# Kernel tuning notes

Hardware: AMD Instinct MI355X
Metric: run time of the kernel (lower is better)

The kernel has to match this reference:

```python
import jax, jax.numpy as jnp
import numpy as np

N, FIN, H, FOUT = 4096, 128, 4, 64
NEG_INF = -1e9


def _xavier(key, shape):
    fan_in, fan_out = shape[-2], shape[-1]
    limit = float(np.sqrt(6.0 / (fan_in + fan_out)))
    return jax.random.uniform(key, shape, jnp.float32, -limit, limit)


def setup_inputs() -> dict:
    key = jax.random.key(0)
    ks = jax.random.split(key, 7)
    x = jax.random.normal(ks[0], (N, FIN), jnp.float32)
    u = jax.random.uniform(ks[1], (N, N))
    mask = jnp.where(u < 0.02, 0.0, NEG_INF).astype(jnp.float32)
    idx = jnp.arange(N)
    mask = mask.at[idx, idx].set(0.0)
    proj_param = _xavier(ks[2], (H, FIN, FOUT))          # per-head projection
    score_src = _xavier(ks[3], (H, FOUT, 1))             # scoring_fn_source (IMP1 layout)
    score_tgt = _xavier(ks[4], (H, FOUT, 1))             # scoring_fn_target
    skip_w = _xavier(ks[5], (H * FOUT, FIN))             # skip_proj Linear weight
    bias = jnp.zeros((H * FOUT,), jnp.float32)
    return {"x": x, "mask": mask, "proj_param": proj_param,
            "score_src": score_src, "score_tgt": score_tgt,
            "skip_w": skip_w, "bias": bias}


def reference(x, mask, proj_param, score_src, score_tgt, skip_w, bias):
    # project: [1,N,Fin] @ [H,Fin,Fout] -> [H,N,Fout]
    h = jnp.einsum('nf,hfo->hno', x, proj_param)
    # additive (Bahdanau-style) scores
    s_src = jnp.matmul(h, score_src)                     # [H,N,1]
    s_tgt = jnp.matmul(h, score_tgt)                     # [H,N,1]
    all_scores = jax.nn.leaky_relu(s_src + jnp.swapaxes(s_tgt, 1, 2), 0.2)  # [H,N,N]
    attn = jax.nn.softmax(all_scores + mask[None, :, :], axis=-1)           # [H,N,N]
    # aggregate: [H,N,N] @ [H,N,Fout] -> [N,H,Fout]
    out = jnp.einsum('hnm,hmo->nho', attn, h)
    # skip connection (dims differ: Fin != H*Fout -> use skip_proj)
    out = out + jnp.matmul(x, skip_w.T).reshape(N, H, FOUT)
    out = out.reshape(N, H * FOUT) + bias                # concat heads + bias
    return jax.nn.elu(out)
```

## Files before the change

kernel.cpp:

```cpp
#include <hip/hip_runtime.h>
#include <hip/hip_bf16.h>
#include <math.h>


#define NN   4096
#define FIN  128
#define NH   4
#define FO   64
#define HF   256
#define SEG  96
#define LIST 192
#define GEMM_BLOCKS 512

typedef unsigned short ushort_t;
typedef unsigned int uint4n __attribute__((ext_vector_type(4)));

__device__ __forceinline__ ushort_t f2bf(float f) {
    __hip_bfloat16 h = __float2bfloat16(f);
    union { __hip_bfloat16 h; ushort_t u; } c; c.h = h; return c.u;
}
__device__ __forceinline__ float bf2f(ushort_t u) {
    union { unsigned int i; float f; } c; c.i = ((unsigned int)u) << 16; return c.f;
}

__global__ __launch_bounds__(256) void k0_gemm(
        const float* __restrict__ x,
        const float* __restrict__ proj,
        const float* __restrict__ skw,
        const float* __restrict__ asrc,
        const float* __restrict__ atgt,
        ushort_t* __restrict__ h2b, float* __restrict__ skip_ws,
        float* __restrict__ src4, float* __restrict__ tgt4) {
    __shared__ float sA[64 * 68];
    __shared__ float sB[64 * 64];
    const int tid = threadIdx.x;
    const int blk = blockIdx.x;

    const int bc = blk >> 6;
    const int i0 = (blk & 63) * 64;
    const int tx = tid & 15, ty = tid >> 4;
    const int r0 = ty << 2, c0 = tx << 2;
    float acc[4][4] = {};

    #pragma unroll
    for (int kb = 0; kb < FIN; kb += 64) {
        if (kb) __syncthreads();
        #pragma unroll
        for (int q = 0; q < 4; q++) {
            int s   = tid + q * 256;
            int row = s >> 4;
            int c4  = (s & 15) << 2;
            float4 v = *(const float4*)(x + (size_t)(i0 + row) * FIN + kb + c4);
            float* d = sA + row * 68 + c4;
            d[0] = v.x; d[1] = v.y; d[2] = v.z; d[3] = v.w;
        }
        if (bc < 4) {
            const float4* src = (const float4*)(proj + (size_t)bc * FIN * FO
                                                + (size_t)kb * FO);
            #pragma unroll
            for (int q = 0; q < 4; q++) {
                int s = tid + q * 256;
                *(float4*)(sB + (size_t)s * 4) = src[s];
            }
        } else {
            const float* sw = skw + (size_t)(bc - 4) * 64 * FIN;
            #pragma unroll
            for (int q = 0; q < 4; q++) {
                int s  = tid + q * 256;
                int c  = s & 63;
                int k4 = (s >> 6) << 2;
                float4 v = *(const float4*)(sw + (size_t)c * FIN + kb + k4);
                sB[(k4 + 0) * 64 + c] = v.x;
                sB[(k4 + 1) * 64 + c] = v.y;
                sB[(k4 + 2) * 64 + c] = v.z;
                sB[(k4 + 3) * 64 + c] = v.w;
            }
        }
        __syncthreads();

        #pragma unroll 2
        for (int k = 0; k < 64; k += 4) {
            alignas(16) float a[4][4];
            alignas(16) float b[4][4];
            #pragma unroll
            for (int rr = 0; rr < 4; rr++)
                *(float4*)a[rr] = *(const float4*)(sA + (r0 + rr) * 68 + k);
            #pragma unroll
            for (int kk = 0; kk < 4; kk++)
                *(float4*)b[kk] = *(const float4*)(sB + (k + kk) * 64 + c0);
            #pragma unroll
            for (int kk = 0; kk < 4; kk++)
                #pragma unroll
                for (int rr = 0; rr < 4; rr++)
                    #pragma unroll
                    for (int cc = 0; cc < 4; cc++)
                        acc[rr][cc] = fmaf(a[rr][kk], b[kk][cc], acc[rr][cc]);
        }
    }

    if (bc < 4) {
        #pragma unroll
        for (int rr = 0; rr < 4; rr++) {
            ushort4 hv;
            hv.x = f2bf(acc[rr][0]); hv.y = f2bf(acc[rr][1]);
            hv.z = f2bf(acc[rr][2]); hv.w = f2bf(acc[rr][3]);
            *(ushort4*)(h2b + (size_t)(i0 + r0 + rr) * HF + bc * 64 + c0) = hv;
        }
        float as[4], at[4];
        #pragma unroll
        for (int cc = 0; cc < 4; cc++) {
            as[cc] = asrc[bc * FO + c0 + cc];
            at[cc] = atgt[bc * FO + c0 + cc];
        }
        #pragma unroll
        for (int rr = 0; rr < 4; rr++) {
            float ps = acc[rr][0] * as[0] + acc[rr][1] * as[1]
                     + acc[rr][2] * as[2] + acc[rr][3] * as[3];
            float pt = acc[rr][0] * at[0] + acc[rr][1] * at[1]
                     + acc[rr][2] * at[2] + acc[rr][3] * at[3];
            #pragma unroll
            for (int off = 8; off >= 1; off >>= 1) {
                ps += __shfl_xor(ps, off, 64);
                pt += __shfl_xor(pt, off, 64);
            }
            if (tx == 0) {
                int i = i0 + r0 + rr;
                src4[(size_t)i * 4 + bc] = ps;
                tgt4[(size_t)i * 4 + bc] = pt;
            }
        }
    } else {
        float* dst = skip_ws + (size_t)i0 * HF + (bc - 4) * 64;
        #pragma unroll
        for (int rr = 0; rr < 4; rr++)
            *(float4*)(dst + (size_t)(r0 + rr) * HF + c0) = *(float4*)acc[rr];
    }
}

__global__ __launch_bounds__(256) void k1_attn(
        const unsigned int* __restrict__ mask,
        const ushort_t* __restrict__ h2b,
        const float* __restrict__ skip_ws,
        const float* __restrict__ src4,
        const float* __restrict__ tgt4,
        const float* __restrict__ bias,
        float* __restrict__ out) {
    __shared__ ushort_t s_seg[4][SEG];
    __shared__ int      s_j[LIST];
    __shared__ float    s_p[4][LIST + 1];
    __shared__ float    s_red[4][256];
    __shared__ int      s_cnt[4];
    __shared__ float    s_inv[4];

    const int tid  = threadIdx.x;
    const int lane = tid & 63, w = tid >> 6;
    const int i    = blockIdx.x;

    const uint4n* mb = (const uint4n*)mask + (size_t)i * 1024;
    uint4n cur[4];
    #pragma unroll
    for (int s = 0; s < 4; s++)
        cur[s] = mb[w * 256 + lane + s * 64];

    const float skipv = skip_ws[(size_t)i * HF + tid];
    const float bv    = bias[tid];
    const float sc    = src4[(size_t)i * 4 + w];

    int base = 0;
    #pragma unroll
    for (int s = 0; s < 4; s++) {
        #pragma unroll
        for (int e = 0; e < 4; e++) {
            bool hit = (cur[s][e] & 0x7fffffffu) == 0u;
            unsigned long long bal = __ballot(hit);
            int pre = __builtin_amdgcn_mbcnt_hi(
                          (unsigned int)(bal >> 32),
                          __builtin_amdgcn_mbcnt_lo((unsigned int)bal, 0));
            if (hit) {
                int slot = base + pre;
                if (slot < SEG)
                    s_seg[w][slot] =
                        (ushort_t)(w * 1024 + s * 256 + lane * 4 + e);
            }
            base += (int)__popcll(bal);
        }
    }
    if (lane == 0) s_cnt[w] = base < SEG ? base : SEG;
    __syncthreads();

    const int t0 = s_cnt[0], t1 = s_cnt[1], t2 = s_cnt[2], t3 = s_cnt[3];
    const int off  = (w > 0 ? t0 : 0) + (w > 1 ? t1 : 0) + (w > 2 ? t2 : 0);
    const int mine = s_cnt[w];
    for (int kk = lane; kk < mine; kk += 64) {
        int pp = off + kk;
        if (pp < LIST) s_j[pp] = s_seg[w][kk];
    }
    int c = t0 + t1 + t2 + t3;
    c = c < LIST ? c : LIST;
    __syncthreads();

    float lsum = 0.f;
    for (int kk = lane; kk < c; kk += 64) {
        int j = s_j[kk];
        float p = sc + tgt4[(size_t)j * 4 + w];
        p = p > 0.f ? p : 0.2f * p;
        p = __expf(p);
        s_p[w][kk] = p;
        lsum += p;
    }
    #pragma unroll
    for (int o = 32; o >= 1; o >>= 1)
        lsum += __shfl_xor(lsum, o, 64);
    if (lane == 0) s_inv[w] = lsum > 0.f ? 1.0f / lsum : 0.0f;
    __syncthreads();

    const int h = lane >> 4;
    const ushort_t* hp = h2b + 4 * lane;
    float4 acc = {0.f, 0.f, 0.f, 0.f};
    int kk = w;
    for (; kk + 4 < c; kk += 8) {
        int   j0 = s_j[kk],        j1 = s_j[kk + 4];
        float p0 = s_p[h][kk],     p1 = s_p[h][kk + 4];
        ushort4 a0 = *(const ushort4*)(hp + (size_t)j0 * HF);
        ushort4 a1 = *(const ushort4*)(hp + (size_t)j1 * HF);
        acc.x = fmaf(p0, bf2f(a0.x), acc.x);
        acc.y = fmaf(p0, bf2f(a0.y), acc.y);
        acc.z = fmaf(p0, bf2f(a0.z), acc.z);
        acc.w = fmaf(p0, bf2f(a0.w), acc.w);
        acc.x = fmaf(p1, bf2f(a1.x), acc.x);
        acc.y = fmaf(p1, bf2f(a1.y), acc.y);
        acc.z = fmaf(p1, bf2f(a1.z), acc.z);
        acc.w = fmaf(p1, bf2f(a1.w), acc.w);
    }
    if (kk < c) {
        int   j0 = s_j[kk];
        float p0 = s_p[h][kk];
        ushort4 a0 = *(const ushort4*)(hp + (size_t)j0 * HF);
        acc.x = fmaf(p0, bf2f(a0.x), acc.x);
        acc.y = fmaf(p0, bf2f(a0.y), acc.y);
        acc.z = fmaf(p0, bf2f(a0.z), acc.z);
        acc.w = fmaf(p0, bf2f(a0.w), acc.w);
    }
    *(float4*)&s_red[w][4 * lane] = acc;
    __syncthreads();

    float tot = s_red[0][tid] + s_red[1][tid] + s_red[2][tid] + s_red[3][tid];
    float vv = tot * s_inv[tid >> 6] + skipv + bv;
    vv = vv > 0.f ? vv : expm1f(vv);
    out[(size_t)i * HF + tid] = vv;
}

extern "C" void kernel_launch(void* const* d_in, const int* in_sizes, int n_in,
                              void* d_out, int out_size, void* d_ws, size_t ws_size,
                              hipStream_t stream) {
    const float*        x    = (const float*)d_in[0];
    const unsigned int* mask = (const unsigned int*)d_in[1];
    const float*        proj = (const float*)d_in[2];
    const float*        asrc = (const float*)d_in[3];
    const float*        atgt = (const float*)d_in[4];
    const float*        skw  = (const float*)d_in[5];
    const float*        bias = (const float*)d_in[6];
    float*              out  = (float*)d_out;

    char* ws = (char*)d_ws;
    ushort_t* h2b     = (ushort_t*)ws;
    float*    skip_ws = (float*)(ws + (2u << 20));
    float*    src4    = (float*)(ws + (6u << 20));
    float*    tgt4    = (float*)(ws + (6u << 20) + (64u << 10));

    hipLaunchKernelGGL(k0_gemm, dim3(GEMM_BLOCKS), dim3(256), 0, stream,
                       x, proj, skw, asrc, atgt,
                       h2b, skip_ws, src4, tgt4);
    hipLaunchKernelGGL(k1_attn, dim3(NN), dim3(256), 0, stream,
                       mask, h2b, skip_ws, src4, tgt4, bias, out);
}
```

Before: 127.1 us.

## Process two rows per block with prefetched mask and bitmask-based compaction

Each attention block now handles two output rows and loads the second row's mask before processing the first, so the mask read overlaps with the first row's gather and compute. Neighbor compaction changes from per-element ballots into a per-wave segment buffer to a per-lane 16-bit hit mask plus a wave prefix scan that writes indices directly into the shared list. The aggregation loop is unrolled to four outstanding gathers. The trade-offs are half as many blocks, fewer waves in flight to hide latency, and more registers held per thread.

```diff
diff --git a/kernel.cpp b/kernel.cpp
--- a/kernel.cpp
+++ b/kernel.cpp
@@ -8,9 +8,9 @@
 #define NH   4
 #define FO   64
 #define HF   256
-#define SEG  96
 #define LIST 192
 #define GEMM_BLOCKS 512
+#define ROWS_PER 2
 
 typedef unsigned short ushort_t;
 typedef unsigned int uint4n __attribute__((ext_vector_type(4)));
@@ -137,6 +137,111 @@
     }
 }
 
+struct K1Shared {
+    int   s_j[LIST];
+    float s_p[4][LIST + 1];
+    float s_red[4][256];
+    int   s_cnt[4];
+    float s_inv[4];
+};
+
+__device__ __forceinline__ void k1_row(
+        K1Shared* sh, unsigned hm, float sc, float skipv, float bv, int i,
+        int tid, int lane, int w,
+        const ushort_t* __restrict__ h2b,
+        const float* __restrict__ tgt4,
+        float* __restrict__ out) {
+    const int cl = __popc(hm);
+    int incl = cl;
+    #pragma unroll
+    for (int o = 1; o < 64; o <<= 1) {
+        int t = __shfl_up(incl, o, 64);
+        if (lane >= o) incl += t;
+    }
+    const int excl = incl - cl;
+    if (lane == 63) sh->s_cnt[w] = incl;
+    __syncthreads();
+    const int t0 = sh->s_cnt[0], t1 = sh->s_cnt[1],
+              t2 = sh->s_cnt[2], t3 = sh->s_cnt[3];
+    const int off = (w > 0 ? t0 : 0) + (w > 1 ? t1 : 0) + (w > 2 ? t2 : 0);
+    int c = t0 + t1 + t2 + t3;
+    c = c < LIST ? c : LIST;
+
+    int p = off + excl;
+    unsigned mm = hm;
+    while (mm) {
+        int b = __builtin_ctz(mm);
+        mm &= mm - 1;
+        if (p < LIST)
+            sh->s_j[p] = (w << 10) + ((b >> 2) << 8) + (lane << 2) + (b & 3);
+        p++;
+    }
+    __syncthreads();
+
+    float lsum = 0.f;
+    for (int kk = lane; kk < c; kk += 64) {
+        int j = sh->s_j[kk];
+        float pv = sc + tgt4[(size_t)j * 4 + w];
+        pv = pv > 0.f ? pv : 0.2f * pv;
+        pv = __expf(pv);
+        sh->s_p[w][kk] = pv;
+        lsum += pv;
+    }
+    #pragma unroll
+    for (int o = 32; o >= 1; o >>= 1)
+        lsum += __shfl_xor(lsum, o, 64);
+    if (lane == 0) sh->s_inv[w] = lsum > 0.f ? 1.0f / lsum : 0.0f;
+    __syncthreads();
+
+    const int h = lane >> 4;
+    const ushort_t* hp = h2b + 4 * lane;
+    float4 acc = {0.f, 0.f, 0.f, 0.f};
+    int kk = w;
+    for (; kk + 12 < c; kk += 16) {
+        int   j0 = sh->s_j[kk],      j1 = sh->s_j[kk + 4];
+        int   j2 = sh->s_j[kk + 8],  j3 = sh->s_j[kk + 12];
+        float p0 = sh->s_p[h][kk],   p1 = sh->s_p[h][kk + 4];
+        float p2 = sh->s_p[h][kk + 8], p3 = sh->s_p[h][kk + 12];
+        ushort4 a0 = *(const ushort4*)(hp + (size_t)j0 * HF);
+        ushort4 a1 = *(const ushort4*)(hp + (size_t)j1 * HF);
+        ushort4 a2 = *(const ushort4*)(hp + (size_t)j2 * HF);
+        ushort4 a3 = *(const ushort4*)(hp + (size_t)j3 * HF);
+        acc.x = fmaf(p0, bf2f(a0.x), acc.x);
+        acc.y = fmaf(p0, bf2f(a0.y), acc.y);
+        acc.z = fmaf(p0, bf2f(a0.z), acc.z);
+        acc.w = fmaf(p0, bf2f(a0.w), acc.w);
+        acc.x = fmaf(p1, bf2f(a1.x), acc.x);
+        acc.y = fmaf(p1, bf2f(a1.y), acc.y);
+        acc.z = fmaf(p1, bf2f(a1.z), acc.z);
+        acc.w = fmaf(p1, bf2f(a1.w), acc.w);
+        acc.x = fmaf(p2, bf2f(a2.x), acc.x);
+        acc.y = fmaf(p2, bf2f(a2.y), acc.y);
+        acc.z = fmaf(p2, bf2f(a2.z), acc.z);
+        acc.w = fmaf(p2, bf2f(a2.w), acc.w);
+        acc.x = fmaf(p3, bf2f(a3.x), acc.x);
+        acc.y = fmaf(p3, bf2f(a3.y), acc.y);
+        acc.z = fmaf(p3, bf2f(a3.z), acc.z);
+        acc.w = fmaf(p3, bf2f(a3.w), acc.w);
+    }
+    for (; kk < c; kk += 4) {
+        int   j0 = sh->s_j[kk];
+        float p0 = sh->s_p[h][kk];
+        ushort4 a0 = *(const ushort4*)(hp + (size_t)j0 * HF);
+        acc.x = fmaf(p0, bf2f(a0.x), acc.x);
+        acc.y = fmaf(p0, bf2f(a0.y), acc.y);
+        acc.z = fmaf(p0, bf2f(a0.z), acc.z);
+        acc.w = fmaf(p0, bf2f(a0.w), acc.w);
+    }
+    *(float4*)&sh->s_red[w][4 * lane] = acc;
+    __syncthreads();
+
+    float tot = sh->s_red[0][tid] + sh->s_red[1][tid]
+              + sh->s_red[2][tid] + sh->s_red[3][tid];
+    float vv = tot * sh->s_inv[tid >> 6] + skipv + bv;
+    vv = vv > 0.f ? vv : expm1f(vv);
+    out[(size_t)i * HF + tid] = vv;
+}
+
 __global__ __launch_bounds__(256) void k1_attn(
         const unsigned int* __restrict__ mask,
         const ushort_t* __restrict__ h2b,
@@ -145,109 +250,45 @@
         const float* __restrict__ tgt4,
         const float* __restrict__ bias,
         float* __restrict__ out) {
-    __shared__ ushort_t s_seg[4][SEG];
-    __shared__ int      s_j[LIST];
-    __shared__ float    s_p[4][LIST + 1];
-    __shared__ float    s_red[4][256];
-    __shared__ int      s_cnt[4];
-    __shared__ float    s_inv[4];
-
+    __shared__ K1Shared sh;
     const int tid  = threadIdx.x;
     const int lane = tid & 63, w = tid >> 6;
-    const int i    = blockIdx.x;
-
-    const uint4n* mb = (const uint4n*)mask + (size_t)i * 1024;
-    uint4n cur[4];
+    const int i0   = blockIdx.x * ROWS_PER;
+
+    const uint4n* mb = (const uint4n*)mask;
+    const size_t base = (size_t)i0 * 1024 + (size_t)(w * 256 + lane);
+    uint4n m0[4];
+    #pragma unroll
+    for (int s = 0; s < 4; s++) m0[s] = mb[base + s * 64];
+
+    const float skip0 = skip_ws[(size_t)i0 * HF + tid];
+    const float skip1 = skip_ws[(size_t)(i0 + 1) * HF + tid];
+    const float bv    = bias[tid];
+    const float sc0   = src4[(size_t)i0 * 4 + w];
+    const float sc1   = src4[(size_t)(i0 + 1) * 4 + w];
+
+    unsigned hm0 = 0;
     #pragma unroll
     for (int s = 0; s < 4; s++)
-        cur[s] = mb[w * 256 + lane + s * 64];
-
-    const float skipv = skip_ws[(size_t)i * HF + tid];
-    const float bv    = bias[tid];
-    const float sc    = src4[(size_t)i * 4 + w];
-
-    int base = 0;
-    #pragma unroll
-    for (int s = 0; s < 4; s++) {
-        #pragma unroll
-        for (int e = 0; e < 4; e++) {
-            bool hit = (cur[s][e] & 0x7fffffffu) == 0u;
-            unsigned long long bal = __ballot(hit);
-            int pre = __builtin_amdgcn_mbcnt_hi(
-                          (unsigned int)(bal >> 32),
-                          __builtin_amdgcn_mbcnt_lo((unsigned int)bal, 0));
-            if (hit) {
-                int slot = base + pre;
-                if (slot < SEG)
-                    s_seg[w][slot] =
-                        (ushort_t)(w * 1024 + s * 256 + lane * 4 + e);
-            }
-            base += (int)__popcll(bal);
-        }
-    }
-    if (lane == 0) s_cnt[w] = base < SEG ? base : SEG;
-    __syncthreads();
-
-    const int t0 = s_cnt[0], t1 = s_cnt[1], t2 = s_cnt[2], t3 = s_cnt[3];
-    const int off  = (w > 0 ? t0 : 0) + (w > 1 ? t1 : 0) + (w > 2 ? t2 : 0);
-    const int mine = s_cnt[w];
-    for (int kk = lane; kk < mine; kk += 64) {
-        int pp = off + kk;
-        if (pp < LIST) s_j[pp] = s_seg[w][kk];
-    }
-    int c = t0 + t1 + t2 + t3;
-    c = c < LIST ? c : LIST;
-    __syncthreads();
-
-    float lsum = 0.f;
-    for (int kk = lane; kk < c; kk += 64) {
-        int j = s_j[kk];
-        float p = sc + tgt4[(size_t)j * 4 + w];
-        p = p > 0.f ? p : 0.2f * p;
-        p = __expf(p);
-        s_p[w][kk] = p;
-        lsum += p;
-    }
-    #pragma unroll
-    for (int o = 32; o >= 1; o >>= 1)
-        lsum += __shfl_xor(lsum, o, 64);
-    if (lane == 0) s_inv[w] = lsum > 0.f ? 1.0f / lsum : 0.0f;
-    __syncthreads();
-
-    const int h = lane >> 4;
-    const ushort_t* hp = h2b + 4 * lane;
-    float4 acc = {0.f, 0.f, 0.f, 0.f};
-    int kk = w;
-    for (; kk + 4 < c; kk += 8) {
-        int   j0 = s_j[kk],        j1 = s_j[kk + 4];
-        float p0 = s_p[h][kk],     p1 = s_p[h][kk + 4];
-        ushort4 a0 = *(const ushort4*)(hp + (size_t)j0 * HF);
-        ushort4 a1 = *(const ushort4*)(hp + (size_t)j1 * HF);
-        acc.x = fmaf(p0, bf2f(a0.x), acc.x);
-        acc.y = fmaf(p0, bf2f(a0.y), acc.y);
-        acc.z = fmaf(p0, bf2f(a0.z), acc.z);
-        acc.w = fmaf(p0, bf2f(a0.w), acc.w);
-        acc.x = fmaf(p1, bf2f(a1.x), acc.x);
-        acc.y = fmaf(p1, bf2f(a1.y), acc.y);
-        acc.z = fmaf(p1, bf2f(a1.z), acc.z);
-        acc.w = fmaf(p1, bf2f(a1.w), acc.w);
-    }
-    if (kk < c) {
-        int   j0 = s_j[kk];
-        float p0 = s_p[h][kk];
-        ushort4 a0 = *(const ushort4*)(hp + (size_t)j0 * HF);
-        acc.x = fmaf(p0, bf2f(a0.x), acc.x);
-        acc.y = fmaf(p0, bf2f(a0.y), acc.y);
-        acc.z = fmaf(p0, bf2f(a0.z), acc.z);
-        acc.w = fmaf(p0, bf2f(a0.w), acc.w);
-    }
-    *(float4*)&s_red[w][4 * lane] = acc;
-    __syncthreads();
-
-    float tot = s_red[0][tid] + s_red[1][tid] + s_red[2][tid] + s_red[3][tid];
-    float vv = tot * s_inv[tid >> 6] + skipv + bv;
-    vv = vv > 0.f ? vv : expm1f(vv);
-    out[(size_t)i * HF + tid] = vv;
+        #pragma unroll
+        for (int e = 0; e < 4; e++)
+            hm0 |= ((m0[s][e] & 0x7fffffffu) == 0u ? 1u : 0u) << (s * 4 + e);
+
+    uint4n m1[4];
+    #pragma unroll
+    for (int s = 0; s < 4; s++) m1[s] = mb[base + 1024 + s * 64];
+
+    k1_row(&sh, hm0, sc0, skip0, bv, i0, tid, lane, w, h2b, tgt4, out);
+    __syncthreads();
+
+    unsigned hm1 = 0;
+    #pragma unroll
+    for (int s = 0; s < 4; s++)
+        #pragma unroll
+        for (int e = 0; e < 4; e++)
+            hm1 |= ((m1[s][e] & 0x7fffffffu) == 0u ? 1u : 0u) << (s * 4 + e);
+
+    k1_row(&sh, hm1, sc1, skip1, bv, i0 + 1, tid, lane, w, h2b, tgt4, out);
 }
 
 extern "C" void kernel_launch(void* const* d_in, const int* in_sizes, int n_in,
@@ -271,6 +312,6 @@
     hipLaunchKernelGGL(k0_gemm, dim3(GEMM_BLOCKS), dim3(256), 0, stream,
                        x, proj, skw, asrc, atgt,
                        h2b, skip_ws, src4, tgt4);
-    hipLaunchKernelGGL(k1_attn, dim3(NN), dim3(256), 0, stream,
+    hipLaunchKernelGGL(k1_attn, dim3(NN / ROWS_PER), dim3(256), 0, stream,
                        mask, h2b, skip_ws, src4, tgt4, bias, out);
 }
```

Measured after the change: 128.7 us. About the same (+1.3%).
